# Kernel tuning notes

Hardware: AMD Instinct MI355X
Metric: run time of the kernel (lower is better)

The kernel has to match this reference:

```python
import jax, jax.numpy as jnp
import numpy as np

MX, MY, MZ = 16, 16, 8  # modes_x, modes_y, modes_z
B, S1, S2, S3, I = 4, 64, 64, 40, 32
HID = 2 * I  # factor * dim


def setup_inputs() -> dict:
    key = jax.random.key(0)
    ks = jax.random.split(key, 14)
    s = 0.05
    d = {}
    d["x"] = jax.random.normal(ks[0], (B, S1, S2, S3, I), jnp.float32)
    # 1x1 Conv1d (in_dim -> in_dim)
    d["w_weight"] = jax.random.normal(ks[1], (I, I), jnp.float32) * s
    d["w_bias"] = jax.random.normal(ks[2], (I,), jnp.float32) * s
    # fourier_weight (positive-mode blocks), stored as (..., 2) real/imag like torch
    d["fw_xy"] = jax.random.normal(ks[3], (I, I, MX, MY, 2), jnp.float32) * s
    d["fw_yz"] = jax.random.normal(ks[4], (I, I, MY, MZ, 2), jnp.float32) * s
    d["fw_xz"] = jax.random.normal(ks[5], (I, I, MX, MZ, 2), jnp.float32) * s
    # fourier_weight2 (negative-mode blocks)
    d["fw2_xy"] = jax.random.normal(ks[6], (I, I, MX, MY, 2), jnp.float32) * s
    d["fw2_yz"] = jax.random.normal(ks[7], (I, I, MY, MZ, 2), jnp.float32) * s
    d["fw2_xz"] = jax.random.normal(ks[8], (I, I, MX, MZ, 2), jnp.float32) * s
    # backcast FeedForward: Linear(I->2I), ReLU, Linear(2I->I)
    d["ff_w0"] = jax.random.normal(ks[9], (HID, I), jnp.float32) * s
    d["ff_b0"] = jax.random.normal(ks[10], (HID,), jnp.float32) * s
    d["ff_w1"] = jax.random.normal(ks[11], (I, HID), jnp.float32) * s
    d["ff_b1"] = jax.random.normal(ks[12], (I,), jnp.float32) * s
    return d


def _cplx(w):
    return w[..., 0] + 1j * w[..., 1]


def _forward_fourier(x, w_weight, w_bias, fw_xy, fw_yz, fw_xz, fw2_xy, fw2_yz, fw2_xz):
    xt = jnp.transpose(x, (0, 4, 1, 2, 3))  # b i x y z
    b_, i_, s1, s2, s3 = xt.shape
    # 1x1 conv branch
    x_w = jnp.einsum('oi,bixyz->boxyz', w_weight, xt) + w_bias[None, :, None, None, None]
    # --- xz branch: rfftn over (x, z), real axis = z ---
    ft = jnp.fft.rfftn(xt, axes=(-3, -1))          # (b,i,s1,s2,s3//2+1)
    Z = s3 // 2 + 1
    out = jnp.zeros(ft.shape, ft.dtype)
    out = out.at[:, :, :MX, :, :MZ].set(
        jnp.einsum('bixyz,ioxz->boxyz', ft[:, :, :MX, :, :MZ], _cplx(fw_xz)))
    out = out.at[:, :, :MX, :, Z - MZ:].set(
        jnp.einsum('bixyz,ioxz->boxyz', ft[:, :, :MX, :, Z - MZ:], _cplx(fw2_xz)))
    xz = jnp.fft.irfftn(out, s=(s1, s3), axes=(-3, -1))
    # --- yz branch: rfftn over (y, z), real axis = z ---
    ft = jnp.fft.rfftn(xt, axes=(-2, -1))          # (b,i,s1,s2,s3//2+1)
    out = jnp.zeros(ft.shape, ft.dtype)
    out = out.at[:, :, :, :MY, :MZ].set(
        jnp.einsum('bixyz,ioyz->boxyz', ft[:, :, :, :MY, :MZ], _cplx(fw_yz)))
    out = out.at[:, :, :, :MY, Z - MZ:].set(
        jnp.einsum('bixyz,ioyz->boxyz', ft[:, :, :, :MY, Z - MZ:], _cplx(fw2_yz)))
    yz = jnp.fft.irfftn(out, s=(s2, s3), axes=(-2, -1))
    # --- xy branch: rfftn over (x, y), real axis = y ---
    ft = jnp.fft.rfftn(xt, axes=(-3, -2))          # (b,i,s1,s2//2+1,s3)
    Y = s2 // 2 + 1
    out = jnp.zeros(ft.shape, ft.dtype)
    out = out.at[:, :, :MX, :MY, :].set(
        jnp.einsum('bixyz,ioxy->boxyz', ft[:, :, :MX, :MY, :], _cplx(fw_xy)))
    out = out.at[:, :, :MX, Y - MY:, :].set(
        jnp.einsum('bixyz,ioxy->boxyz', ft[:, :, :MX, Y - MY:, :], _cplx(fw2_xy)))
    xy = jnp.fft.irfftn(out, s=(s1, s2), axes=(-3, -2))
    total = xy + yz + xz + x_w
    return jnp.transpose(total, (0, 2, 3, 4, 1))  # b s1 s2 s3 i


def reference(x, w_weight, w_bias, fw_xy, fw_yz, fw_xz, fw2_xy, fw2_yz, fw2_xz,
              ff_w0, ff_b0, ff_w1, ff_b1):
    h = _forward_fourier(x, w_weight, w_bias, fw_xy, fw_yz, fw_xz, fw2_xy, fw2_yz, fw2_xz)
    # backcast FeedForward (dropout=0, no layer_norm): Linear -> ReLU -> Linear
    h1 = jax.nn.relu(h @ ff_w0.T + ff_b0)
    b = h1 @ ff_w1.T + ff_b1
    return b
```

## Files before the change

### kernel.cpp

```cpp
#include <hip/hip_runtime.h>
#include <math.h>

#define TWO_PI 6.28318530717958647692f
#define NXD 64
#define NYD 64
#define NZD 40
#define CID 32
#define NJZ 16
#define NJY 32

#define R1SLOT 2621440ll
#define R2SLOT 655360ll
#define R3SLOT 2621440ll

typedef __attribute__((ext_vector_type(8))) short short8;
typedef __attribute__((ext_vector_type(4))) float float4v;

__device__ inline unsigned short f2bf(float f) {
  unsigned u = __builtin_bit_cast(unsigned, f);
  unsigned r = (u + 0x7fffu + ((u >> 16) & 1u)) >> 16;
  return (unsigned short)r;
}
__device__ inline float bf2f(unsigned short h) {
  return __builtin_bit_cast(float, (unsigned)h << 16);
}

__device__ __align__(16) unsigned short g_invyAH[2][4][64][8];
__device__ __align__(16) unsigned short g_invyAL[2][4][64][8];
__device__ __align__(16) unsigned short g_invzAH[3][64][8];
__device__ __align__(16) unsigned short g_invzAL[3][64][8];
__device__ __align__(16) unsigned short g_fwdyB[2][4][64][8];
__device__ __align__(16) float2 g_ztw[NJZ][NZD];

__global__ __launch_bounds__(256) void k_twprep() {
  int t = threadIdx.x;
  if (blockIdx.x == 0) {
    for (int idx = t; idx < 2 * 4 * 64 * 8; idx += 256) {
      int j = idx & 7, lane = (idx >> 3) & 63, yt = (idx >> 9) & 3, kt = idx >> 11;
      int l15 = lane & 15, quad = lane >> 4;
      int y = yt * 16 + l15;
      int k = kt * 32 + quad * 8 + j;
      int jy = k >> 1, part = k & 1;
      int ky = (jy < 16) ? jy : jy + 1;
      float s_, c_; sincosf(TWO_PI * ((ky * y) & 63) / 64.0f, &s_, &c_);
      float cj = (ky == 0 || ky == 32) ? 1.0f : 2.0f;
      cj *= (1.0f / 4096.0f);
      float val = part ? -cj * s_ : cj * c_;
      unsigned short h = f2bf(val);
      g_invyAH[kt][yt][lane][j] = h;
      g_invyAL[kt][yt][lane][j] = f2bf(val - bf2f(h));
    }
  } else if (blockIdx.x == 1) {
    for (int idx = t; idx < 2 * 4 * 64 * 8; idx += 256) {
      int j = idx & 7, lane = (idx >> 3) & 63, nt = (idx >> 9) & 3, kt = idx >> 11;
      int l15 = lane & 15, quad = lane >> 4;
      int n = nt * 16 + l15;
      int jy = n >> 1, part = n & 1;
      int ky = (jy < 16) ? jy : jy + 1;
      int y = kt * 32 + quad * 8 + j;
      float s_, c_; sincosf(TWO_PI * ((ky * y) & 63) / 64.0f, &s_, &c_);
      g_fwdyB[kt][nt][lane][j] = f2bf(part ? -s_ : c_);
    }
  } else if (blockIdx.x == 2) {
    for (int idx = t; idx < 3 * 64 * 8; idx += 256) {
      int j = idx & 7, lane = (idx >> 3) & 63, zt = idx >> 9;
      int l15 = lane & 15, quad = lane >> 4;
      int z = zt * 16 + l15;
      int k = quad * 8 + j;
      int jz = k >> 1, part = k & 1;
      int kz = (jz < 8) ? jz : jz + 5;
      float s_, c_; sincosf(TWO_PI * ((kz * z) % 40) / 40.0f, &s_, &c_);
      float cj = (kz == 0 || kz == 20) ? 1.0f : 2.0f;
      cj *= (1.0f / 2560.0f);
      float val = part ? -cj * s_ : cj * c_;
      unsigned short h = f2bf(val);
      g_invzAH[zt][lane][j] = h;
      g_invzAL[zt][lane][j] = f2bf(val - bf2f(h));
    }
  } else {
    for (int k = t; k < NJZ * NZD; k += 256) {
      int j = k / NZD, z = k % NZD;
      int kz = (j < 8) ? j : j + 5;
      int m = (kz * z) % NZD;
      float s_, c_; sincosf(TWO_PI * m / (float)NZD, &s_, &c_);
      g_ztw[j][z] = make_float2(c_, -s_);
    }
  }
}

__global__ __launch_bounds__(256) void k_conv_mfma(const float* __restrict__ X,
    const float* __restrict__ Wc, const float* __restrict__ bias,
    float* __restrict__ out) {
  int t = threadIdx.x;
  int wid = t >> 6, lane = t & 63;
  int l15 = lane & 15, quad = lane >> 4;
  short8 B[2];
  float bb[2];
  for (int nt = 0; nt < 2; ++nt) {
    int o = nt * 16 + l15;
    for (int j = 0; j < 8; ++j) B[nt][j] = (short)f2bf(Wc[o * 32 + quad * 8 + j]);
    bb[nt] = bias[o];
  }
  const int TOT = 40960;
  int wg = blockIdx.x * 4 + wid;
  for (int tt = wg; tt < TOT; tt += gridDim.x * 4) {
    long r0 = (long)tt * 16;
    const float4v* p = (const float4v*)(X + (r0 + l15) * 32 + quad * 8);
    float4v x0 = p[0], x1 = p[1];
    short8 a;
    for (int j = 0; j < 4; ++j) { a[j] = (short)f2bf(x0[j]); a[4 + j] = (short)f2bf(x1[j]); }
    for (int nt = 0; nt < 2; ++nt) {
      float4v acc = {0.f, 0.f, 0.f, 0.f};
      acc = __builtin_amdgcn_mfma_f32_16x16x32_bf16(a, B[nt], acc, 0, 0, 0);
      for (int r = 0; r < 4; ++r)
        out[(r0 + quad * 4 + r) * 32 + nt * 16 + l15] = acc[r] + bb[nt];
    }
  }
}

__global__ __launch_bounds__(512) void k_zproj(const float* __restrict__ X,
    float2* __restrict__ Tb, int b0) {
  __shared__ float xs[4][NZD][CID];
  __shared__ float2 tw[NJZ][NZD];
  int t = threadIdx.x;
  int xy0 = blockIdx.x * 4;
  int b = b0 + blockIdx.z;
  float2* T = Tb + (long)blockIdx.z * R1SLOT;
  const float* src = X + ((long)(b * 4096 + xy0)) * NZD * CID;
  for (int u = 0; u < 4; ++u)
    for (int k = t; k < NZD * CID; k += 512)
      xs[u][k >> 5][k & 31] = src[u * (NZD * CID) + k];
  {
    const float2* gt = &g_ztw[0][0];
    for (int k = t; k < NJZ * NZD; k += 512) tw[k / NZD][k % NZD] = gt[k];
  }
  __syncthreads();
  int j = t >> 5, i = t & 31;
  float2 acc0 = make_float2(0.f, 0.f), acc1 = make_float2(0.f, 0.f);
  float2 acc2 = make_float2(0.f, 0.f), acc3 = make_float2(0.f, 0.f);
  for (int z = 0; z < NZD; ++z) {
    float2 w = tw[j][z];
    float v0 = xs[0][z][i], v1 = xs[1][z][i], v2 = xs[2][z][i], v3 = xs[3][z][i];
    acc0.x += v0 * w.x; acc0.y += v0 * w.y;
    acc1.x += v1 * w.x; acc1.y += v1 * w.y;
    acc2.x += v2 * w.x; acc2.y += v2 * w.y;
    acc3.x += v3 * w.x; acc3.y += v3 * w.y;
  }
  T[((long)(xy0 + 0) * NJZ + j) * CID + i] = acc0;
  T[((long)(xy0 + 1) * NJZ + j) * CID + i] = acc1;
  T[((long)(xy0 + 2) * NJZ + j) * CID + i] = acc2;
  T[((long)(xy0 + 3) * NJZ + j) * CID + i] = acc3;
}

__global__ __launch_bounds__(256) void k_fwddft(const float2* __restrict__ inb,
    float2* __restrict__ Ub, long CS, long SS, long JS) {
  __shared__ float2 tw[64];
  int t = threadIdx.x;
  if (t < 64) {
    float s_, c_; sincosf(TWO_PI * t / 64.0f, &s_, &c_);
    tw[t] = make_float2(c_, -s_);
  }
  int j = blockIdx.x >> 1, mh = blockIdx.x & 1, sc = blockIdx.y;
  int J = gridDim.x >> 1, SD = gridDim.y * 8;
  int m0 = mh * 8;
  int s = sc * 8 + (t >> 5), i = t & 31;
  const float2* in = inb + (long)blockIdx.z * R1SLOT + (long)j * JS + (long)s * SS + i;
  float2 acc[8];
#pragma unroll
  for (int m = 0; m < 8; ++m) acc[m] = make_float2(0.f, 0.f);
  __syncthreads();
#pragma unroll 4
  for (int c = 0; c < 64; ++c) {
    float2 v = in[(long)c * CS];
#pragma unroll
    for (int m = 0; m < 8; ++m) {
      float2 w = tw[((m0 + m) * c) & 63];
      acc[m].x += v.x * w.x - v.y * w.y;
      acc[m].y += v.x * w.y + v.y * w.x;
    }
  }
  float2* U = Ub + (long)blockIdx.z * R3SLOT;
#pragma unroll
  for (int m = 0; m < 8; ++m)
    U[((long)((m0 + m) * J + j) * SD + s) * 32 + i] = acc[m];
}

__global__ __launch_bounds__(256) void k_mix(const float2* __restrict__ Ub,
    float2* __restrict__ Vb, const float* __restrict__ fw, const float* __restrict__ fw2,
    int jsplit, int JW, long OM, long OJ, long OS, int SD) {
  __shared__ float2 Us[64][32];
  __shared__ float2 Wm[32][32];
  int m = blockIdx.x, j = blockIdx.y, t = threadIdx.x;
  int J = gridDim.y;
  const float2* U = Ub + (long)blockIdx.z * R3SLOT + (long)(m * J + j) * SD * 32;
  for (int k = t; k < SD * 32; k += 256) Us[k >> 5][k & 31] = U[k];
  {
    const float* src = (j < jsplit) ? fw : fw2;
    int jl = (j < jsplit) ? j : j - jsplit;
    for (int k = t; k < 1024; k += 256) {
      int i = k >> 5, o = k & 31;
      const float* p = src + (((i * 32 + o) * 16 + m) * JW + jl) * 2;
      Wm[i][o] = make_float2(p[0], p[1]);
    }
  }
  __syncthreads();
  int o = t & 31, sg = t >> 5;
  float2* V = Vb + (long)blockIdx.z * R2SLOT;
  for (int s = sg; s < SD; s += 8) {
    float2 acc = make_float2(0.f, 0.f);
    for (int i2 = 0; i2 < 32; ++i2) {
      float2 u = Us[s][i2], w = Wm[i2][o];
      acc.x += u.x * w.x - u.y * w.y;
      acc.y += u.x * w.y + u.y * w.x;
    }
    V[(long)m * OM + (long)j * OJ + (long)s * OS + o] = acc;
  }
}

__global__ __launch_bounds__(256) void k_invaxis(const float2* __restrict__ Vb,
    float2* __restrict__ Pb) {
  __shared__ float2 Vs[16][CID];
  __shared__ float2 twp[64];
  int s = blockIdx.x, j = blockIdx.y, t = threadIdx.x;
  const float2* V = Vb + (long)blockIdx.z * R2SLOT;
  float2* P = Pb + (long)blockIdx.z * R3SLOT;
  if (t < 64) {
    float s_, c_; sincosf(TWO_PI * t / 64.0f, &s_, &c_);
    twp[t] = make_float2(c_, s_);
  }
  for (int k = t; k < 512; k += 256) {
    int mm = k >> 5, o = k & 31;
    Vs[mm][o] = V[((long)(mm * 64 + s) * NJZ + j) * CID + o];
  }
  __syncthreads();
  int o = t & 31, vg = t >> 5;
  for (int k = 0; k < 8; ++k) {
    int v = vg + 8 * k;
    float2 acc = make_float2(0.f, 0.f);
    for (int mm = 0; mm < 16; ++mm) {
      float2 w = twp[(mm * v) & 63];
      float2 vv = Vs[mm][o];
      acc.x += vv.x * w.x - vv.y * w.y;
      acc.y += vv.x * w.y + vv.y * w.x;
    }
    P[((long)(v * 64 + s) * NJZ + j) * CID + o] = acc;
  }
}

__global__ __launch_bounds__(256) void k_invzadd_mfma(const float2* __restrict__ Pb,
    float* __restrict__ out, long strideV, long strideS, int b0) {
  __shared__ __align__(16) char smem[21504];
  unsigned (*PsH)[21] = (unsigned(*)[21])smem;
  unsigned (*PsL)[21] = (unsigned(*)[21])(smem + 10752);
  float (*Cs)[132] = (float(*)[132])smem;
  int t = threadIdx.x;
  int wid = t >> 6, lane = t & 63;
  int l15 = lane & 15, quad = lane >> 4;
  int b = b0 + blockIdx.z;
  int vv = blockIdx.y;
  int s0 = blockIdx.x * 4;
  short8 AH[3], AL[3];
  for (int zt = 0; zt < 3; ++zt) {
    AH[zt] = *(const short8*)&g_invzAH[zt][lane][0];
    AL[zt] = *(const short8*)&g_invzAL[zt][lane][0];
  }
  const float2* src = Pb + (long)blockIdx.z * R3SLOT + ((long)(vv * 64 + s0) * NJZ) * CID;
  for (int kk = t; kk < 16 * 128; kk += 256) {
    int j = kk >> 7, m = kk & 127;
    int sl = m >> 5, o = m & 31;
    float2 v = src[((long)sl * NJZ + j) * CID + o];
    unsigned short hx = f2bf(v.x), hy = f2bf(v.y);
    unsigned short lx = f2bf(v.x - bf2f(hx)), ly = f2bf(v.y - bf2f(hy));
    PsH[m][j] = (unsigned)hx | ((unsigned)hy << 16);
    PsL[m][j] = (unsigned)lx | ((unsigned)ly << 16);
  }
  __syncthreads();
  short8 bh[2], bl[2];
  for (int mt = 0; mt < 2; ++mt) {
    int mc = wid * 32 + mt * 16 + l15;
    union { unsigned u[4]; short8 s; } th, tl;
    for (int c = 0; c < 4; ++c) {
      th.u[c] = PsH[mc][quad * 4 + c];
      tl.u[c] = PsL[mc][quad * 4 + c];
    }
    bh[mt] = th.s; bl[mt] = tl.s;
  }
  __syncthreads();
  for (int mt = 0; mt < 2; ++mt) {
    int mc = wid * 32 + mt * 16;
    for (int zt = 0; zt < 3; ++zt) {
      float4v acc = {0.f, 0.f, 0.f, 0.f};
      acc = __builtin_amdgcn_mfma_f32_16x16x32_bf16(AL[zt], bh[mt], acc, 0, 0, 0);
      acc = __builtin_amdgcn_mfma_f32_16x16x32_bf16(AH[zt], bl[mt], acc, 0, 0, 0);
      acc = __builtin_amdgcn_mfma_f32_16x16x32_bf16(AH[zt], bh[mt], acc, 0, 0, 0);
      for (int r = 0; r < 4; ++r) {
        int z = zt * 16 + quad * 4 + r;
        if (z < 40) Cs[z][mc + l15] = acc[r];
      }
    }
  }
  __syncthreads();
  float* obb = out + (long)b * (NXD * NYD * NZD * CID) + (long)vv * strideV
             + (long)s0 * strideS;
  for (int idx = t; idx < 4 * 40 * 8; idx += 256) {
    int sl = idx / 320, rem = idx - sl * 320;
    int z = rem >> 3, o4 = rem & 7;
    float4v* gp = (float4v*)(obb + (long)sl * strideS + z * 32 + o4 * 4);
    float4v g = *gp;
    float4v c = *(const float4v*)&Cs[z][sl * 32 + o4 * 4];
    g.x += c.x; g.y += c.y; g.z += c.z; g.w += c.w;
    *gp = g;
  }
}

__global__ __launch_bounds__(256) void k_fwdy_mfma(const float* __restrict__ X,
    float2* __restrict__ Sb, int b0) {
  __shared__ __align__(16) char smem[35328];
  unsigned (*Xs)[37] = (unsigned(*)[37])smem;
  float (*Cs)[69] = (float(*)[69])smem;
  int t = threadIdx.x;
  int wid = t >> 6, lane = t & 63;
  int l15 = lane & 15, quad = lane >> 4;
  int b = b0 + blockIdx.z;
  int x = blockIdx.y;
  int m0 = blockIdx.x * 128;
  short8 Bf[2][4];
  for (int kt = 0; kt < 2; ++kt)
    for (int nt = 0; nt < 4; ++nt)
      Bf[kt][nt] = *(const short8*)&g_fwdyB[kt][nt][lane][0];
  const float* src = X + (((long)b * 64 + x) * 64) * 1280 + m0;
  for (int k = t; k < 32 * 128; k += 256) {
    int y2 = k >> 7, m = k & 127;
    float v0 = src[(long)(2 * y2) * 1280 + m];
    float v1 = src[(long)(2 * y2 + 1) * 1280 + m];
    Xs[m][y2] = (unsigned)f2bf(v0) | ((unsigned)f2bf(v1) << 16);
  }
  __syncthreads();
  short8 a[2][2];
  for (int mt = 0; mt < 2; ++mt) {
    int mrow = wid * 32 + mt * 16 + l15;
    for (int kt = 0; kt < 2; ++kt) {
      union { unsigned u[4]; short8 s; } tmp;
      for (int c = 0; c < 4; ++c) tmp.u[c] = Xs[mrow][kt * 16 + quad * 4 + c];
      a[mt][kt] = tmp.s;
    }
  }
  __syncthreads();
  for (int mt = 0; mt < 2; ++mt) {
    for (int nt = 0; nt < 4; ++nt) {
      float4v acc = {0.f, 0.f, 0.f, 0.f};
      acc = __builtin_amdgcn_mfma_f32_16x16x32_bf16(a[mt][0], Bf[0][nt], acc, 0, 0, 0);
      acc = __builtin_amdgcn_mfma_f32_16x16x32_bf16(a[mt][1], Bf[1][nt], acc, 0, 0, 0);
      int n = nt * 16 + l15;
      for (int r = 0; r < 4; ++r)
        Cs[wid * 32 + mt * 16 + quad * 4 + r][n] = acc[r];
    }
  }
  __syncthreads();
  float2* S = Sb + (long)blockIdx.z * R1SLOT + (long)x * (NJY * NZD * CID) + m0;
  for (int idx = t; idx < 32 * 128; idx += 256) {
    int jy = idx >> 7, m = idx & 127;
    S[(long)jy * 1280 + m] = make_float2(Cs[m][2 * jy], Cs[m][2 * jy + 1]);
  }
}

__global__ __launch_bounds__(256) void k_invx_xy(const float2* __restrict__ V2b,
    float2* __restrict__ P2b) {
  __shared__ float2 Vs[16][CID];
  __shared__ float2 twp[64];
  int jy = blockIdx.x, z = blockIdx.y, t = threadIdx.x;
  const float2* V2 = V2b + (long)blockIdx.z * R2SLOT;
  float2* P2 = P2b + (long)blockIdx.z * R3SLOT;
  if (t < 64) {
    float s_, c_; sincosf(TWO_PI * t / 64.0f, &s_, &c_);
    twp[t] = make_float2(c_, s_);
  }
  for (int k = t; k < 512; k += 256) {
    int kx = k >> 5, o = k & 31;
    Vs[kx][o] = V2[(((long)kx * NJY + jy) * NZD + z) * CID + o];
  }
  __syncthreads();
  int o = t & 31, xg = t >> 5;
  for (int k = 0; k < 8; ++k) {
    int x = xg + 8 * k;
    float2 acc = make_float2(0.f, 0.f);
    for (int kx = 0; kx < 16; ++kx) {
      float2 w = twp[(kx * x) & 63];
      float2 v = Vs[kx][o];
      acc.x += v.x * w.x - v.y * w.y;
      acc.y += v.x * w.y + v.y * w.x;
    }
    P2[(((long)x * NJY + jy) * NZD + z) * CID + o] = acc;
  }
}

__global__ __launch_bounds__(256) void k_invyadd_mfma(const float2* __restrict__ P2b,
    float* __restrict__ out, int b0) {
  __shared__ __align__(16) char smem[18944];
  unsigned (*PsH)[37] = (unsigned(*)[37])smem;
  unsigned (*PsL)[37] = (unsigned(*)[37])(smem + 9472);
  float (*Cs)[68] = (float(*)[68])smem;
  int t = threadIdx.x;
  int wid = t >> 6, lane = t & 63;
  int l15 = lane & 15, quad = lane >> 4;
  int b = b0 + blockIdx.z;
  int x = blockIdx.y;
  int m0 = blockIdx.x * 64;
  const float2* src = P2b + (long)blockIdx.z * R3SLOT + (long)x * (NJY * NZD * CID) + m0;
  for (int kk = t; kk < 32 * 64; kk += 256) {
    int jy = kk >> 6, m = kk & 63;
    float2 v = src[(long)jy * (NZD * CID) + m];
    unsigned short hx = f2bf(v.x), hy = f2bf(v.y);
    unsigned short lx = f2bf(v.x - bf2f(hx)), ly = f2bf(v.y - bf2f(hy));
    PsH[m][jy] = (unsigned)hx | ((unsigned)hy << 16);
    PsL[m][jy] = (unsigned)lx | ((unsigned)ly << 16);
  }
  __syncthreads();
  int mc = wid * 16;
  short8 bh0, bh1, bl0, bl1;
  {
    union { unsigned u[4]; short8 s; } t0, t1, t2, t3;
    for (int c = 0; c < 4; ++c) {
      t0.u[c] = PsH[mc + l15][quad * 4 + c];
      t1.u[c] = PsH[mc + l15][16 + quad * 4 + c];
      t2.u[c] = PsL[mc + l15][quad * 4 + c];
      t3.u[c] = PsL[mc + l15][16 + quad * 4 + c];
    }
    bh0 = t0.s; bh1 = t1.s; bl0 = t2.s; bl1 = t3.s;
  }
  __syncthreads();
#pragma unroll 1
  for (int yt = 0; yt < 4; ++yt) {
    short8 AH0 = *(const short8*)&g_invyAH[0][yt][lane][0];
    short8 AH1 = *(const short8*)&g_invyAH[1][yt][lane][0];
    short8 AL0 = *(const short8*)&g_invyAL[0][yt][lane][0];
    short8 AL1 = *(const short8*)&g_invyAL[1][yt][lane][0];
    float4v acc = {0.f, 0.f, 0.f, 0.f};
    acc = __builtin_amdgcn_mfma_f32_16x16x32_bf16(AL0, bh0, acc, 0, 0, 0);
    acc = __builtin_amdgcn_mfma_f32_16x16x32_bf16(AL1, bh1, acc, 0, 0, 0);
    acc = __builtin_amdgcn_mfma_f32_16x16x32_bf16(AH0, bl0, acc, 0, 0, 0);
    acc = __builtin_amdgcn_mfma_f32_16x16x32_bf16(AH1, bl1, acc, 0, 0, 0);
    acc = __builtin_amdgcn_mfma_f32_16x16x32_bf16(AH0, bh0, acc, 0, 0, 0);
    acc = __builtin_amdgcn_mfma_f32_16x16x32_bf16(AH1, bh1, acc, 0, 0, 0);
    for (int r = 0; r < 4; ++r) {
      int y = yt * 16 + quad * 4 + r;
      Cs[y][mc + l15] = acc[r];
    }
  }
  __syncthreads();
  float* ob = out + ((long)(b * 64 + x)) * (NYD * NZD * CID) + m0;
  for (int idx = t; idx < 64 * 16; idx += 256) {
    int y = idx >> 4, f = idx & 15;
    float4v* gp = (float4v*)(ob + (long)y * (NZD * CID) + f * 4);
    float4v g = *gp;
    float4v c = *(const float4v*)&Cs[y][f * 4];
    g.x += c.x; g.y += c.y; g.z += c.z; g.w += c.w;
    *gp = g;
  }
}

__global__ __launch_bounds__(256) void k_ff_mfma(float* __restrict__ out,
    const float* __restrict__ W0, const float* __restrict__ b0,
    const float* __restrict__ W1, const float* __restrict__ b1) {
  __shared__ unsigned short h1s[4][16 * 64];
  int t = threadIdx.x;
  int wid = t >> 6, lane = t & 63;
  int l15 = lane & 15, quad = lane >> 4;
  short8 B1[4];
  float bb0[4];
  for (int nt = 0; nt < 4; ++nt) {
    int hh = nt * 16 + l15;
    for (int j = 0; j < 8; ++j) B1[nt][j] = (short)f2bf(W0[hh * 32 + quad * 8 + j]);
    bb0[nt] = b0[hh];
  }
  short8 B2[2][2];
  float bb1[2];
  for (int k0 = 0; k0 < 2; ++k0)
    for (int nt = 0; nt < 2; ++nt) {
      int o = nt * 16 + l15;
      for (int j = 0; j < 8; ++j)
        B2[k0][nt][j] = (short)f2bf(W1[o * 64 + k0 * 32 + quad * 8 + j]);
    }
  for (int nt = 0; nt < 2; ++nt) bb1[nt] = b1[nt * 16 + l15];

  const int TOT = 40960;
  int wg = blockIdx.x * 4 + wid;
  unsigned short* hs = h1s[wid];
  for (int tt = wg; tt < TOT; tt += gridDim.x * 4) {
    long r0 = (long)tt * 16;
    const float4v* p = (const float4v*)(out + (r0 + l15) * 32 + quad * 8);
    float4v x0 = p[0], x1 = p[1];
    short8 a1;
    for (int j = 0; j < 4; ++j) { a1[j] = (short)f2bf(x0[j]); a1[4 + j] = (short)f2bf(x1[j]); }
    for (int nt = 0; nt < 4; ++nt) {
      float4v acc = {0.f, 0.f, 0.f, 0.f};
      acc = __builtin_amdgcn_mfma_f32_16x16x32_bf16(a1, B1[nt], acc, 0, 0, 0);
      for (int r = 0; r < 4; ++r) {
        float v = acc[r] + bb0[nt];
        v = v > 0.f ? v : 0.f;
        hs[(quad * 4 + r) * 64 + nt * 16 + l15] = f2bf(v);
      }
    }
    short8 a2[2];
    for (int k0 = 0; k0 < 2; ++k0)
      a2[k0] = *(const short8*)&hs[l15 * 64 + k0 * 32 + quad * 8];
    for (int nt = 0; nt < 2; ++nt) {
      float4v acc = {0.f, 0.f, 0.f, 0.f};
      acc = __builtin_amdgcn_mfma_f32_16x16x32_bf16(a2[0], B2[0][nt], acc, 0, 0, 0);
      acc = __builtin_amdgcn_mfma_f32_16x16x32_bf16(a2[1], B2[1][nt], acc, 0, 0, 0);
      for (int r = 0; r < 4; ++r)
        out[(r0 + quad * 4 + r) * 32 + nt * 16 + l15] = acc[r] + bb1[nt];
    }
  }
}

extern "C" void kernel_launch(void* const* d_in, const int* in_sizes, int n_in,
                              void* d_out, int out_size, void* d_ws, size_t ws_size,
                              hipStream_t stream) {
  const float* X       = (const float*)d_in[0];
  const float* w_w     = (const float*)d_in[1];
  const float* w_b     = (const float*)d_in[2];
  const float* fw_xy   = (const float*)d_in[3];
  const float* fw_yz   = (const float*)d_in[4];
  const float* fw_xz   = (const float*)d_in[5];
  const float* fw2_xy  = (const float*)d_in[6];
  const float* fw2_yz  = (const float*)d_in[7];
  const float* fw2_xz  = (const float*)d_in[8];
  const float* ff_w0   = (const float*)d_in[9];
  const float* ff_b0   = (const float*)d_in[10];
  const float* ff_w1   = (const float*)d_in[11];
  const float* ff_b1   = (const float*)d_in[12];
  float* out = (float*)d_out;
  char* ws = (char*)d_ws;

  const size_t need_full = (size_t)(R1SLOT + R2SLOT + R3SLOT) * 4 * 8;
  bool full = ws_size >= need_full;

  float2 *r1, *r2, *r3;
  if (full) {
    r1 = (float2*)ws;
    r2 = (float2*)(ws + (size_t)R1SLOT * 4 * 8);
    r3 = (float2*)(ws + (size_t)(R1SLOT + R2SLOT) * 4 * 8);
  } else {
    r1 = (float2*)ws;
    r2 = (float2*)(ws + (size_t)R1SLOT * 8);
    r3 = (float2*)(ws + (size_t)(R1SLOT + R2SLOT) * 8);
  }

  k_twprep<<<dim3(4), dim3(256), 0, stream>>>();
  k_conv_mfma<<<dim3(2560), dim3(256), 0, stream>>>(X, w_w, w_b, out);

  int nz = full ? 4 : 1;
  int nb = full ? 1 : 4;
  for (int b = 0; b < nb; ++b) {
    k_zproj<<<dim3(1024, 1, nz), dim3(512), 0, stream>>>(X, r1, b);
    k_fwddft<<<dim3(32, 8, nz), dim3(256), 0, stream>>>(r1, r3, 32768, 512, 32);
    k_mix<<<dim3(16, 16, nz), dim3(256), 0, stream>>>(r3, r2, fw_xz, fw2_xz,
        8, 8, 32768, 32, 512, 64);
    k_invaxis<<<dim3(64, 16, nz), dim3(256), 0, stream>>>(r2, r3);
    k_invzadd_mfma<<<dim3(16, 64, nz), dim3(256), 0, stream>>>(r3, out, 64 * 40 * 32, 40 * 32, b);
    k_fwddft<<<dim3(32, 8, nz), dim3(256), 0, stream>>>(r1, r3, 512, 32768, 32);
    k_mix<<<dim3(16, 16, nz), dim3(256), 0, stream>>>(r3, r2, fw_yz, fw2_yz,
        8, 8, 32768, 32, 512, 64);
    k_invaxis<<<dim3(64, 16, nz), dim3(256), 0, stream>>>(r2, r3);
    k_invzadd_mfma<<<dim3(16, 64, nz), dim3(256), 0, stream>>>(r3, out, 40 * 32, 64 * 40 * 32, b);
    k_fwdy_mfma<<<dim3(10, 64, nz), dim3(256), 0, stream>>>(X, r1, b);
    k_fwddft<<<dim3(64, 5, nz), dim3(256), 0, stream>>>(r1, r3, 40960, 32, 1280);
    k_mix<<<dim3(16, 32, nz), dim3(256), 0, stream>>>(r3, r2, fw_xy, fw2_xy,
        16, 16, 40960, 1280, 32, 40);
    k_invx_xy<<<dim3(32, 40, nz), dim3(256), 0, stream>>>(r2, r3);
    k_invyadd_mfma<<<dim3(20, 64, nz), dim3(256), 0, stream>>>(r3, out, b);
  }

  k_ff_mfma<<<dim3(2560), dim3(256), 0, stream>>>(out, ff_w0, ff_b0, ff_w1, ff_b1);
}
```

Measured before the change: 728.3 us.

## Fuse 1x1 conv into z-projection kernel and split forward DFT modes finer

The standalone 1x1 conv MFMA kernel is folded into k_zproj, which already stages the x tile in shared memory. The conv now reads from that staged tile instead of re-reading X from global memory, which removes one full pass over the input and one kernel launch. The shared tile is padded to 33 columns to reduce bank conflicts. Separately, k_fwddft now computes 4 modes per block instead of 8 with twice as many blocks, raising parallelism at the cost of reading the input more times.

```diff
diff --git a/kernel.cpp b/kernel.cpp
--- a/kernel.cpp
+++ b/kernel.cpp
@@ -88,41 +88,14 @@
   }
 }
 
-__global__ __launch_bounds__(256) void k_conv_mfma(const float* __restrict__ X,
-    const float* __restrict__ Wc, const float* __restrict__ bias,
-    float* __restrict__ out) {
+__global__ __launch_bounds__(512) void k_zproj(const float* __restrict__ X,
+    float2* __restrict__ Tb, const float* __restrict__ Wc,
+    const float* __restrict__ bias, float* __restrict__ out, int b0) {
+  __shared__ float xs[4][NZD][33];
+  __shared__ float2 tw[NJZ][NZD];
   int t = threadIdx.x;
   int wid = t >> 6, lane = t & 63;
   int l15 = lane & 15, quad = lane >> 4;
-  short8 B[2];
-  float bb[2];
-  for (int nt = 0; nt < 2; ++nt) {
-    int o = nt * 16 + l15;
-    for (int j = 0; j < 8; ++j) B[nt][j] = (short)f2bf(Wc[o * 32 + quad * 8 + j]);
-    bb[nt] = bias[o];
-  }
-  const int TOT = 40960;
-  int wg = blockIdx.x * 4 + wid;
-  for (int tt = wg; tt < TOT; tt += gridDim.x * 4) {
-    long r0 = (long)tt * 16;
-    const float4v* p = (const float4v*)(X + (r0 + l15) * 32 + quad * 8);
-    float4v x0 = p[0], x1 = p[1];
-    short8 a;
-    for (int j = 0; j < 4; ++j) { a[j] = (short)f2bf(x0[j]); a[4 + j] = (short)f2bf(x1[j]); }
-    for (int nt = 0; nt < 2; ++nt) {
-      float4v acc = {0.f, 0.f, 0.f, 0.f};
-      acc = __builtin_amdgcn_mfma_f32_16x16x32_bf16(a, B[nt], acc, 0, 0, 0);
-      for (int r = 0; r < 4; ++r)
-        out[(r0 + quad * 4 + r) * 32 + nt * 16 + l15] = acc[r] + bb[nt];
-    }
-  }
-}
-
-__global__ __launch_bounds__(512) void k_zproj(const float* __restrict__ X,
-    float2* __restrict__ Tb, int b0) {
-  __shared__ float xs[4][NZD][CID];
-  __shared__ float2 tw[NJZ][NZD];
-  int t = threadIdx.x;
   int xy0 = blockIdx.x * 4;
   int b = b0 + blockIdx.z;
   float2* T = Tb + (long)blockIdx.z * R1SLOT;
@@ -134,22 +107,47 @@
     const float2* gt = &g_ztw[0][0];
     for (int k = t; k < NJZ * NZD; k += 512) tw[k / NZD][k % NZD] = gt[k];
   }
-  __syncthreads();
-  int j = t >> 5, i = t & 31;
-  float2 acc0 = make_float2(0.f, 0.f), acc1 = make_float2(0.f, 0.f);
-  float2 acc2 = make_float2(0.f, 0.f), acc3 = make_float2(0.f, 0.f);
-  for (int z = 0; z < NZD; ++z) {
-    float2 w = tw[j][z];
-    float v0 = xs[0][z][i], v1 = xs[1][z][i], v2 = xs[2][z][i], v3 = xs[3][z][i];
-    acc0.x += v0 * w.x; acc0.y += v0 * w.y;
-    acc1.x += v1 * w.x; acc1.y += v1 * w.y;
-    acc2.x += v2 * w.x; acc2.y += v2 * w.y;
-    acc3.x += v3 * w.x; acc3.y += v3 * w.y;
-  }
-  T[((long)(xy0 + 0) * NJZ + j) * CID + i] = acc0;
-  T[((long)(xy0 + 1) * NJZ + j) * CID + i] = acc1;
-  T[((long)(xy0 + 2) * NJZ + j) * CID + i] = acc2;
-  T[((long)(xy0 + 3) * NJZ + j) * CID + i] = acc3;
+  short8 Bc[2];
+  float bb[2];
+  for (int nt = 0; nt < 2; ++nt) {
+    int o = nt * 16 + l15;
+    for (int j = 0; j < 8; ++j) Bc[nt][j] = (short)f2bf(Wc[o * 32 + quad * 8 + j]);
+    bb[nt] = bias[o];
+  }
+  __syncthreads();
+  {
+    int j = t >> 5, i = t & 31;
+    float2 acc0 = make_float2(0.f, 0.f), acc1 = make_float2(0.f, 0.f);
+    float2 acc2 = make_float2(0.f, 0.f), acc3 = make_float2(0.f, 0.f);
+    for (int z = 0; z < NZD; ++z) {
+      float2 w = tw[j][z];
+      float v0 = xs[0][z][i], v1 = xs[1][z][i], v2 = xs[2][z][i], v3 = xs[3][z][i];
+      acc0.x += v0 * w.x; acc0.y += v0 * w.y;
+      acc1.x += v1 * w.x; acc1.y += v1 * w.y;
+      acc2.x += v2 * w.x; acc2.y += v2 * w.y;
+      acc3.x += v3 * w.x; acc3.y += v3 * w.y;
+    }
+    T[((long)(xy0 + 0) * NJZ + j) * CID + i] = acc0;
+    T[((long)(xy0 + 1) * NJZ + j) * CID + i] = acc1;
+    T[((long)(xy0 + 2) * NJZ + j) * CID + i] = acc2;
+    T[((long)(xy0 + 3) * NJZ + j) * CID + i] = acc3;
+  }
+  float* ob = out + ((long)(b * 4096 + xy0)) * NZD * CID;
+  for (int tile = wid; tile < 10; tile += 8) {
+    int rr = tile * 16 + l15;
+    int u = rr / NZD, z = rr % NZD;
+    short8 a;
+    for (int j = 0; j < 8; ++j) a[j] = (short)f2bf(xs[u][z][quad * 8 + j]);
+    for (int nt = 0; nt < 2; ++nt) {
+      float4v acc = {0.f, 0.f, 0.f, 0.f};
+      acc = __builtin_amdgcn_mfma_f32_16x16x32_bf16(a, Bc[nt], acc, 0, 0, 0);
+      for (int r = 0; r < 4; ++r) {
+        int rg = tile * 16 + quad * 4 + r;
+        int uu = rg / NZD, zz = rg % NZD;
+        ob[(long)uu * (NZD * CID) + zz * CID + nt * 16 + l15] = acc[r] + bb[nt];
+      }
+    }
+  }
 }
 
 __global__ __launch_bounds__(256) void k_fwddft(const float2* __restrict__ inb,
@@ -160,20 +158,20 @@
     float s_, c_; sincosf(TWO_PI * t / 64.0f, &s_, &c_);
     tw[t] = make_float2(c_, -s_);
   }
-  int j = blockIdx.x >> 1, mh = blockIdx.x & 1, sc = blockIdx.y;
-  int J = gridDim.x >> 1, SD = gridDim.y * 8;
-  int m0 = mh * 8;
+  int j = blockIdx.x >> 2, mq = blockIdx.x & 3, sc = blockIdx.y;
+  int J = gridDim.x >> 2, SD = gridDim.y * 8;
+  int m0 = mq * 4;
   int s = sc * 8 + (t >> 5), i = t & 31;
   const float2* in = inb + (long)blockIdx.z * R1SLOT + (long)j * JS + (long)s * SS + i;
-  float2 acc[8];
+  float2 acc[4];
 #pragma unroll
-  for (int m = 0; m < 8; ++m) acc[m] = make_float2(0.f, 0.f);
+  for (int m = 0; m < 4; ++m) acc[m] = make_float2(0.f, 0.f);
   __syncthreads();
 #pragma unroll 4
   for (int c = 0; c < 64; ++c) {
     float2 v = in[(long)c * CS];
 #pragma unroll
-    for (int m = 0; m < 8; ++m) {
+    for (int m = 0; m < 4; ++m) {
       float2 w = tw[((m0 + m) * c) & 63];
       acc[m].x += v.x * w.x - v.y * w.y;
       acc[m].y += v.x * w.y + v.y * w.x;
@@ -181,7 +179,7 @@
   }
   float2* U = Ub + (long)blockIdx.z * R3SLOT;
 #pragma unroll
-  for (int m = 0; m < 8; ++m)
+  for (int m = 0; m < 4; ++m)
     U[((long)((m0 + m) * J + j) * SD + s) * 32 + i] = acc[m];
 }
 
@@ -548,24 +546,23 @@
   }
 
   k_twprep<<<dim3(4), dim3(256), 0, stream>>>();
-  k_conv_mfma<<<dim3(2560), dim3(256), 0, stream>>>(X, w_w, w_b, out);
 
   int nz = full ? 4 : 1;
   int nb = full ? 1 : 4;
   for (int b = 0; b < nb; ++b) {
-    k_zproj<<<dim3(1024, 1, nz), dim3(512), 0, stream>>>(X, r1, b);
-    k_fwddft<<<dim3(32, 8, nz), dim3(256), 0, stream>>>(r1, r3, 32768, 512, 32);
+    k_zproj<<<dim3(1024, 1, nz), dim3(512), 0, stream>>>(X, r1, w_w, w_b, out, b);
+    k_fwddft<<<dim3(64, 8, nz), dim3(256), 0, stream>>>(r1, r3, 32768, 512, 32);
     k_mix<<<dim3(16, 16, nz), dim3(256), 0, stream>>>(r3, r2, fw_xz, fw2_xz,
         8, 8, 32768, 32, 512, 64);
     k_invaxis<<<dim3(64, 16, nz), dim3(256), 0, stream>>>(r2, r3);
     k_invzadd_mfma<<<dim3(16, 64, nz), dim3(256), 0, stream>>>(r3, out, 64 * 40 * 32, 40 * 32, b);
-    k_fwddft<<<dim3(32, 8, nz), dim3(256), 0, stream>>>(r1, r3, 512, 32768, 32);
+    k_fwddft<<<dim3(64, 8, nz), dim3(256), 0, stream>>>(r1, r3, 512, 32768, 32);
     k_mix<<<dim3(16, 16, nz), dim3(256), 0, stream>>>(r3, r2, fw_yz, fw2_yz,
         8, 8, 32768, 32, 512, 64);
     k_invaxis<<<dim3(64, 16, nz), dim3(256), 0, stream>>>(r2, r3);
     k_invzadd_mfma<<<dim3(16, 64, nz), dim3(256), 0, stream>>>(r3, out, 40 * 32, 64 * 40 * 32, b);
     k_fwdy_mfma<<<dim3(10, 64, nz), dim3(256), 0, stream>>>(X, r1, b);
-    k_fwddft<<<dim3(64, 5, nz), dim3(256), 0, stream>>>(r1, r3, 40960, 32, 1280);
+    k_fwddft<<<dim3(128, 5, nz), dim3(256), 0, stream>>>(r1, r3, 40960, 32, 1280);
     k_mix<<<dim3(16, 32, nz), dim3(256), 0, stream>>>(r3, r2, fw_xy, fw2_xy,
         16, 16, 40960, 1280, 32, 40);
     k_invx_xy<<<dim3(32, 40, nz), dim3(256), 0, stream>>>(r2, r3);
```

New measurement: 754.0 us. 3.5% more time.
